# Optimization experiments

Hardware: AMD Instinct MI355X
Metric: run time of the kernel (lower is better)

## Reference

```python
import jax, jax.numpy as jnp
import numpy as np

D_MODEL = 1024
D_FF = 4096
NUM_EXPERTS = 8
TOP_K = 2
B, S = 4, 4096


def setup_inputs() -> dict:
    key = jax.random.key(0)
    ks = jax.random.split(key, 7)
    s_dm = 1.0 / np.sqrt(D_MODEL)
    s_ff = 1.0 / np.sqrt(D_FF)
    return {
        "x": jax.random.normal(ks[0], (B, S, D_MODEL), jnp.float32),
        "router_w": jax.random.normal(ks[1], (D_MODEL, NUM_EXPERTS), jnp.float32) * s_dm,
        "router_b": jnp.zeros((NUM_EXPERTS,), jnp.float32),
        "w1": jax.random.normal(ks[2], (NUM_EXPERTS, D_MODEL, D_FF), jnp.float32) * s_dm,
        "b1": jnp.zeros((NUM_EXPERTS, D_FF), jnp.float32),
        "w2": jax.random.normal(ks[3], (NUM_EXPERTS, D_FF, D_MODEL), jnp.float32) * s_ff,
        "b2": jnp.zeros((NUM_EXPERTS, D_MODEL), jnp.float32),
    }


def reference(x, router_w, router_b, w1, b1, w2, b2):
    Bx, Sx, D = x.shape
    xf = x.reshape(-1, D)  # [T, D], T = B*S
    # Router: top-k logits -> softmax over the k selected experts
    logits = xf @ router_w + router_b            # [T, E]
    top_w, sel = jax.lax.top_k(logits, TOP_K)    # [T, k], [T, k]
    gates = jax.nn.softmax(top_w, axis=-1)       # [T, k]

    def body(i, acc):
        # Dense expert FFN over all tokens; gate is zero for tokens not routed
        # to expert i, which reproduces the masked gather/scatter combine exactly.
        h = jax.nn.gelu(xf @ w1[i] + b1[i], approximate=False)  # [T, d_ff]
        out_i = h @ w2[i] + b2[i]                               # [T, D]
        gate_i = jnp.sum(gates * (sel == i), axis=-1, keepdims=True)  # [T, 1]
        return acc + out_i * gate_i

    out = jax.lax.fori_loop(0, NUM_EXPERTS, body, jnp.zeros_like(xf))
    return out.reshape(Bx, Sx, D)
```

## Files before the change

kernel.cpp:

```cpp
#include <hip/hip_runtime.h>

#define D_MODEL 1024
#define D_FF    4096
#define NE      8
#define T_TOK   16384
#define HOFF    (2u * 1024u * 1024u)

using frag_ab = __attribute__((ext_vector_type(8))) short;
using f32x4   = __attribute__((ext_vector_type(4))) float;
using ushort8 = __attribute__((ext_vector_type(8))) unsigned short;
using ushort4v = __attribute__((ext_vector_type(4))) unsigned short;

__device__ __forceinline__ unsigned short f2bf(float f) {
  unsigned int u = __builtin_bit_cast(unsigned int, f);
  u += 0x7FFFu + ((u >> 16) & 1u);
  return (unsigned short)(u >> 16);
}
__device__ __forceinline__ float bf2f(unsigned short s) {
  unsigned int u = ((unsigned int)s) << 16;
  return __builtin_bit_cast(float, u);
}

__device__ __forceinline__ float gelu_f(float v) {
  float z  = v * 0.70710678118654752f;
  float az = __builtin_fabsf(z);
  float d  = __builtin_fmaf(0.3275911f, az, 1.0f);
  float t;
  asm("v_rcp_f32_e32 %0, %1" : "=v"(t) : "v"(d));
  t = t * (2.0f - d * t);
  float p = __builtin_fmaf(t, 1.061405429f, -1.453152027f);
  p = __builtin_fmaf(t, p, 1.421413741f);
  p = __builtin_fmaf(t, p, -0.284496736f);
  p = __builtin_fmaf(t, p, 0.254829592f);
  p = p * t;
  float ex = __expf(-az * az);
  float er = __builtin_fmaf(-p, ex, 1.0f);
  unsigned int su = __builtin_bit_cast(unsigned int, z) & 0x80000000u;
  er = __builtin_bit_cast(float, __builtin_bit_cast(unsigned int, er) | su);
  return 0.5f * v * (1.0f + er);
}

__device__ __forceinline__ void gload16(const void* g, void* l) {
  __builtin_amdgcn_global_load_lds((const __attribute__((address_space(1))) void*)g,
                                   (__attribute__((address_space(3))) void*)l, 16, 0, 0);
}

#define FENCE __builtin_amdgcn_sched_barrier(0)
#define BARRIER do { FENCE; __builtin_amdgcn_s_barrier(); FENCE; } while (0)
__device__ __forceinline__ void waitv(int n) {
  if (n == 6) asm volatile("s_waitcnt vmcnt(6)" ::: "memory");
  else        asm volatile("s_waitcnt vmcnt(0)" ::: "memory");
}

__global__ __launch_bounds__(256) void router_kernel(
    const float* __restrict__ x, const float* __restrict__ rw,
    const float* __restrict__ rb, int* __restrict__ cnt,
    int* __restrict__ tok, int* __restrict__ mi, float* __restrict__ mg,
    unsigned short* __restrict__ xb) {
  __shared__ int lcnt[NE];
  __shared__ int base[NE];
  __shared__ int lexp[64][2];
  __shared__ int lrank[64][2];
  int w = threadIdx.x >> 6, lane = threadIdx.x & 63;
  if (threadIdx.x < NE) lcnt[threadIdx.x] = 0;
  __syncthreads();

  for (int it = 0; it < 16; ++it) {
    int li = w * 16 + it;
    int t = blockIdx.x * 64 + li;
    const float* xr = x + (size_t)t * D_MODEL;
    unsigned short* xbr = xb + (size_t)t * D_MODEL;
    double acc[NE];
#pragma unroll
    for (int e = 0; e < NE; ++e) acc[e] = 0.0;
#pragma unroll
    for (int it2 = 0; it2 < 4; ++it2) {
      int j = it2 * 256 + lane * 4;
      float4 v = *(const float4*)(xr + j);
      ushort4v o;
      o[0] = f2bf(v.x); o[1] = f2bf(v.y); o[2] = f2bf(v.z); o[3] = f2bf(v.w);
      *(ushort4v*)(xbr + j) = o;
      const float* w0 = rw + (size_t)j * NE;
      const float vv[4] = {v.x, v.y, v.z, v.w};
#pragma unroll
      for (int q = 0; q < 4; ++q) {
        double xv = (double)vv[q];
#pragma unroll
        for (int e = 0; e < NE; ++e) acc[e] += xv * (double)w0[q * NE + e];
      }
    }
#pragma unroll
    for (int e = 0; e < NE; ++e) {
      double v = acc[e];
#pragma unroll
      for (int s = 32; s > 0; s >>= 1) v += __shfl_xor(v, s, 64);
      acc[e] = v;
    }
    if (lane == 0) {
      double lg[NE];
#pragma unroll
      for (int e = 0; e < NE; ++e) lg[e] = acc[e] + (double)rb[e];
      int b0 = 0; double v0 = lg[0];
#pragma unroll
      for (int e = 1; e < NE; ++e) if (lg[e] > v0) { v0 = lg[e]; b0 = e; }
      int b1 = -1; double v1 = -1.0e300;
#pragma unroll
      for (int e = 0; e < NE; ++e) if (e != b0 && lg[e] > v1) { v1 = lg[e]; b1 = e; }
      double g0 = 1.0 / (1.0 + exp(v1 - v0));
      lexp[li][0] = b0; lexp[li][1] = b1;
      lrank[li][0] = atomicAdd(&lcnt[b0], 1);
      lrank[li][1] = atomicAdd(&lcnt[b1], 1);
      mg[2 * t + 0] = (float)g0; mg[2 * t + 1] = (float)(1.0 - g0);
    }
  }
  __syncthreads();
  if (threadIdx.x < NE) base[threadIdx.x] = atomicAdd(&cnt[threadIdx.x], lcnt[threadIdx.x]);
  __syncthreads();
  if (threadIdx.x < 64) {
    int li = threadIdx.x;
    int t = blockIdx.x * 64 + li;
    int e0 = lexp[li][0], e1 = lexp[li][1];
    int p0 = base[e0] + lrank[li][0], p1 = base[e1] + lrank[li][1];
    tok[e0 * T_TOK + p0] = t;
    tok[e1 * T_TOK + p1] = t;
    mi[4 * t + 0] = e0; mi[4 * t + 1] = e1;
    mi[4 * t + 2] = p0; mi[4 * t + 3] = p1;
  }
}

__global__ __launch_bounds__(256) void transpose_cvt_kernel(const float* __restrict__ in,
                                                            unsigned short* __restrict__ out,
                                                            int R, int C) {
  __shared__ unsigned short tile[64][66];
  int e = blockIdx.z;
  int r0 = blockIdx.y * 64, c0 = blockIdx.x * 64;
  int t = threadIdx.x;
  int rr = t >> 4, cc = (t & 15) * 4;
  const float* src = in + ((size_t)e * R + r0) * C + c0;
#pragma unroll
  for (int p = 0; p < 4; ++p) {
    int r = rr + p * 16;
    float4 v = *(const float4*)(src + (size_t)r * C + cc);
    tile[r][cc + 0] = f2bf(v.x);
    tile[r][cc + 1] = f2bf(v.y);
    tile[r][cc + 2] = f2bf(v.z);
    tile[r][cc + 3] = f2bf(v.w);
  }
  __syncthreads();
  int oc = t >> 2, kc = (t & 3) * 16;
  ushort8 v0, v1;
#pragma unroll
  for (int i = 0; i < 8; ++i) v0[i] = tile[kc + i][oc];
#pragma unroll
  for (int i = 0; i < 8; ++i) v1[i] = tile[kc + 8 + i][oc];
  unsigned short* dst = out + ((size_t)e * C + c0 + oc) * R + r0 + kc;
  *(ushort8*)dst = v0;
  *(ushort8*)(dst + 8) = v1;
}

__device__ __forceinline__ int find_tile256(const int* __restrict__ cnt, int slot,
                                            int& e, int& lt, int& ne, int& hb) {
  int tacc = 0, base = 0;
  for (int i = 0; i < NE; ++i) {
    int n = cnt[i];
    int tl = (n + 255) >> 8;
    if (slot < tacc + tl) { e = i; lt = slot - tacc; ne = n; hb = base; return 1; }
    tacc += tl; base += tl << 8;
  }
  return 0;
}

#define STG_A(qa, kt, b) do { \
    gload16(pA##qa##0 + (size_t)(kt) * 64, ldsp + (b) * 65536 + dA + (qa) * 8192); \
    gload16(pA##qa##1 + (size_t)(kt) * 64, ldsp + (b) * 65536 + dA + (qa) * 8192 + 16384); \
  } while (0)
#define STG_B(qb, kt, b) do { \
    gload16(pB##qb##0 + (size_t)(kt) * 64, ldsp + (b) * 65536 + 32768 + dB + (qb) * 4096); \
    gload16(pB##qb##1 + (size_t)(kt) * 64, ldsp + (b) * 65536 + 32768 + dB + (qb) * 4096 + 16384); \
  } while (0)

#define GEMM_BODY(NTILES)                                                        \
  f32x4 acc[8][4] = {};                                                          \
  frag_ab a[4][2], bb[4][2];                                                     \
  const int NT = (NTILES);                                                       \
  STG_A(0, 0, 0); STG_B(0, 0, 0); STG_B(1, 0, 0); STG_A(1, 0, 0);                \
  STG_A(0, 1, 1); STG_B(0, 1, 1); STG_B(1, 1, 1);                                \
  waitv(6); BARRIER;                                                             \
  for (int t = 0; t < NT; ++t) {                                                 \
    const char* AB = ldsp + (t & 1) * 65536;                                     \
    _Pragma("unroll") for (int i = 0; i < 4; ++i) {                              \
      a[i][0] = *(const frag_ab*)(AB + aoff + i * 2048 + xs0);                   \
      a[i][1] = *(const frag_ab*)(AB + aoff + i * 2048 + xs1);                   \
    }                                                                            \
    _Pragma("unroll") for (int j = 0; j < 2; ++j) {                              \
      bb[j][0] = *(const frag_ab*)(AB + boff + j * 2048 + xs0);                  \
      bb[j][1] = *(const frag_ab*)(AB + boff + j * 2048 + xs1);                  \
    }                                                                            \
    if (t + 1 < NT) STG_A(1, t + 1, (t + 1) & 1);                                \
    BARRIER;                                                                     \
    __builtin_amdgcn_s_setprio(1);                                               \
    _Pragma("unroll") for (int i = 0; i < 4; ++i)                                \
      _Pragma("unroll") for (int j = 0; j < 2; ++j) {                            \
        acc[i][j] = __builtin_amdgcn_mfma_f32_16x16x32_bf16(a[i][0], bb[j][0], acc[i][j], 0, 0, 0); \
        acc[i][j] = __builtin_amdgcn_mfma_f32_16x16x32_bf16(a[i][1], bb[j][1], acc[i][j], 0, 0, 0); \
      }                                                                          \
    __builtin_amdgcn_s_setprio(0);                                               \
    BARRIER;                                                                     \
    _Pragma("unroll") for (int j = 0; j < 2; ++j) {                              \
      bb[2 + j][0] = *(const frag_ab*)(AB + boff + (2 + j) * 2048 + xs0);        \
      bb[2 + j][1] = *(const frag_ab*)(AB + boff + (2 + j) * 2048 + xs1);        \
    }                                                                            \
    if (t + 2 < NT) STG_A(0, t + 2, t & 1);                                      \
    BARRIER;                                                                     \
    __builtin_amdgcn_s_setprio(1);                                               \
    _Pragma("unroll") for (int i = 0; i < 4; ++i)                                \
      _Pragma("unroll") for (int j = 0; j < 2; ++j) {                            \
        acc[i][2 + j] = __builtin_amdgcn_mfma_f32_16x16x32_bf16(a[i][0], bb[2 + j][0], acc[i][2 + j], 0, 0, 0); \
        acc[i][2 + j] = __builtin_amdgcn_mfma_f32_16x16x32_bf16(a[i][1], bb[2 + j][1], acc[i][2 + j], 0, 0, 0); \
      }                                                                          \
    __builtin_amdgcn_s_setprio(0);                                               \
    BARRIER;                                                                     \
    _Pragma("unroll") for (int i = 0; i < 4; ++i) {                              \
      a[i][0] = *(const frag_ab*)(AB + aoff + 8192 + i * 2048 + xs0);            \
      a[i][1] = *(const frag_ab*)(AB + aoff + 8192 + i * 2048 + xs1);            \
    }                                                                            \
    if (t + 2 < NT) STG_B(0, t + 2, t & 1);                                      \
    BARRIER;                                                                     \
    __builtin_amdgcn_s_setprio(1);                                               \
    _Pragma("unroll") for (int i = 0; i < 4; ++i)                                \
      _Pragma("unroll") for (int j = 0; j < 2; ++j) {                            \
        acc[4 + i][2 + j] = __builtin_amdgcn_mfma_f32_16x16x32_bf16(a[i][0], bb[2 + j][0], acc[4 + i][2 + j], 0, 0, 0); \
        acc[4 + i][2 + j] = __builtin_amdgcn_mfma_f32_16x16x32_bf16(a[i][1], bb[2 + j][1], acc[4 + i][2 + j], 0, 0, 0); \
      }                                                                          \
    __builtin_amdgcn_s_setprio(0);                                               \
    BARRIER;                                                                     \
    if (t + 2 < NT) STG_B(1, t + 2, t & 1);                                      \
    BARRIER;                                                                     \
    __builtin_amdgcn_s_setprio(1);                                               \
    _Pragma("unroll") for (int i = 0; i < 4; ++i)                                \
      _Pragma("unroll") for (int j = 0; j < 2; ++j) {                            \
        acc[4 + i][j] = __builtin_amdgcn_mfma_f32_16x16x32_bf16(a[i][0], bb[j][0], acc[4 + i][j], 0, 0, 0); \
        acc[4 + i][j] = __builtin_amdgcn_mfma_f32_16x16x32_bf16(a[i][1], bb[j][1], acc[4 + i][j], 0, 0, 0); \
      }                                                                          \
    __builtin_amdgcn_s_setprio(0);                                               \
    waitv((t + 2 < NT) ? 6 : 0);                                                 \
    BARRIER;                                                                     \
  }

__global__ __launch_bounds__(512, 2) void gemm1_kernel(
    const unsigned short* __restrict__ xb, const unsigned short* __restrict__ w1t,
    const float* __restrict__ b1, const int* __restrict__ cnt, const int* __restrict__ tok,
    unsigned short* __restrict__ H) {
  __shared__ __align__(16) char lds[131072];
  int bid = blockIdx.x;
  int s = bid >> 3;
  int tt = (bid & 7) + 8 * (s >> 4);
  int e, lt, ne, hb;
  if (!find_tile256(cnt, tt, e, lt, ne, hb)) return;
  char* ldsp = (char*)lds;
  const int tid = threadIdx.x;
  const int lane = tid & 63, w = tid >> 6;
  const int wm = w >> 2, wn = w & 3;
  const int r16 = lane & 15, kg = lane >> 4;
  const int n0 = (s & 15) * 256;

  const int xs0 = (kg ^ (r16 & 7)) * 16;
  const int xs1 = ((4 + kg) ^ (r16 & 7)) * 16;
  const int aoff = (wm * 128 + r16) * 128;
  const int boff = 32768 + (wn * 64 + r16) * 128;

  const int v = w * 8 + (lane >> 3);
  const int c8off = ((lane & 7) ^ ((lane >> 3) & 7)) * 8;
  const int dA = w * 1024;
  const int dB = (w & 3) * 1024 + (w >> 2) * 8192;
  const int tokbase = e * T_TOK;
  int rA00 = v, rA01 = v + 128, rA10 = 64 + v, rA11 = 192 + v;
  int g00 = lt * 256 + rA00, g01 = lt * 256 + rA01, g10 = lt * 256 + rA10, g11 = lt * 256 + rA11;
  int tk00 = tok[tokbase + ((g00 < ne) ? g00 : 0)];
  int tk01 = tok[tokbase + ((g01 < ne) ? g01 : 0)];
  int tk10 = tok[tokbase + ((g10 < ne) ? g10 : 0)];
  int tk11 = tok[tokbase + ((g11 < ne) ? g11 : 0)];
  const unsigned short* pA00 = xb + (size_t)tk00 * D_MODEL + c8off;
  const unsigned short* pA01 = xb + (size_t)tk01 * D_MODEL + c8off;
  const unsigned short* pA10 = xb + (size_t)tk10 * D_MODEL + c8off;
  const unsigned short* pA11 = xb + (size_t)tk11 * D_MODEL + c8off;
  int rB00 = (v & 31) + (v >> 5) * 64;
  int rB01 = rB00 + 128, rB10 = rB00 + 32, rB11 = rB00 + 160;
  const unsigned short* pB00 = w1t + ((size_t)e * D_FF + n0 + rB00) * D_MODEL + c8off;
  const unsigned short* pB01 = w1t + ((size_t)e * D_FF + n0 + rB01) * D_MODEL + c8off;
  const unsigned short* pB10 = w1t + ((size_t)e * D_FF + n0 + rB10) * D_MODEL + c8off;
  const unsigned short* pB11 = w1t + ((size_t)e * D_FF + n0 + rB11) * D_MODEL + c8off;

  GEMM_BODY(D_MODEL / 64)

  unsigned short (*hlds)[272] = (unsigned short (*)[272])ldsp;
  float b1v[4];
#pragma unroll
  for (int j = 0; j < 4; ++j)
    b1v[j] = b1[e * D_FF + n0 + wn * 64 + j * 16 + r16];
#pragma unroll
  for (int ih = 0; ih < 2; ++ih) {
    if (ih) BARRIER;
#pragma unroll
    for (int i2 = 0; i2 < 4; ++i2)
#pragma unroll
      for (int jj = 0; jj < 4; ++jj) {
        int rl = wm * 64 + i2 * 16 + kg * 4 + jj;
#pragma unroll
        for (int j = 0; j < 4; ++j) {
          int col = wn * 64 + j * 16 + r16;
          int pos = (((col >> 3) ^ (rl & 7)) << 3) | (col & 7);
          hlds[rl][pos] = f2bf(gelu_f(acc[ih * 4 + i2][j][jj] + b1v[j]));
        }
      }
    BARRIER;
    int lrow = tid >> 2, cq = tid & 3;
    int grow = (lrow >> 6) * 128 + ih * 64 + (lrow & 63);
    unsigned short* hdst = H + (size_t)(hb + lt * 256 + grow) * D_FF + n0 + cq * 8;
#pragma unroll
    for (int c = 0; c < 8; ++c) {
      int k = cq + c * 4;
      ushort8 vv = *(const ushort8*)&hlds[lrow][(k ^ (lrow & 7)) << 3];
      __builtin_nontemporal_store(vv, (ushort8*)(hdst + c * 32));
    }
  }
}

__global__ __launch_bounds__(512, 2) void gemm2_kernel(
    const unsigned short* __restrict__ H, const unsigned short* __restrict__ w2t,
    const float* __restrict__ b2, const int* __restrict__ cnt,
    unsigned short* __restrict__ Y) {
  __shared__ __align__(16) char lds[131072];
  int bid = blockIdx.x;
  int s = bid >> 3;
  int tt = (bid & 7) + 8 * (s >> 2);
  int e, lt, ne, hb;
  if (!find_tile256(cnt, tt, e, lt, ne, hb)) return;
  char* ldsp = (char*)lds;
  const int tid = threadIdx.x;
  const int lane = tid & 63, w = tid >> 6;
  const int wm = w >> 2, wn = w & 3;
  const int r16 = lane & 15, kg = lane >> 4;
  const int n0 = (s & 3) * 256;

  const int xs0 = (kg ^ (r16 & 7)) * 16;
  const int xs1 = ((4 + kg) ^ (r16 & 7)) * 16;
  const int aoff = (wm * 128 + r16) * 128;
  const int boff = 32768 + (wn * 64 + r16) * 128;

  const int v = w * 8 + (lane >> 3);
  const int c8off = ((lane & 7) ^ ((lane >> 3) & 7)) * 8;
  const int dA = w * 1024;
  const int dB = (w & 3) * 1024 + (w >> 2) * 8192;
  int rA00 = v, rA01 = v + 128, rA10 = 64 + v, rA11 = 192 + v;
  const unsigned short* pA00 = H + (size_t)(hb + lt * 256 + rA00) * D_FF + c8off;
  const unsigned short* pA01 = H + (size_t)(hb + lt * 256 + rA01) * D_FF + c8off;
  const unsigned short* pA10 = H + (size_t)(hb + lt * 256 + rA10) * D_FF + c8off;
  const unsigned short* pA11 = H + (size_t)(hb + lt * 256 + rA11) * D_FF + c8off;
  int rB00 = (v & 31) + (v >> 5) * 64;
  int rB01 = rB00 + 128, rB10 = rB00 + 32, rB11 = rB00 + 160;
  const unsigned short* pB00 = w2t + ((size_t)e * D_MODEL + n0 + rB00) * D_FF + c8off;
  const unsigned short* pB01 = w2t + ((size_t)e * D_MODEL + n0 + rB01) * D_FF + c8off;
  const unsigned short* pB10 = w2t + ((size_t)e * D_MODEL + n0 + rB10) * D_FF + c8off;
  const unsigned short* pB11 = w2t + ((size_t)e * D_MODEL + n0 + rB11) * D_FF + c8off;

  GEMM_BODY(D_FF / 64)

  unsigned short (*hlds)[272] = (unsigned short (*)[272])ldsp;
  float b2v[4];
#pragma unroll
  for (int j = 0; j < 4; ++j)
    b2v[j] = b2[e * D_MODEL + n0 + wn * 64 + j * 16 + r16];
#pragma unroll
  for (int ih = 0; ih < 2; ++ih) {
    if (ih) BARRIER;
#pragma unroll
    for (int i2 = 0; i2 < 4; ++i2)
#pragma unroll
      for (int jj = 0; jj < 4; ++jj) {
        int rl = wm * 64 + i2 * 16 + kg * 4 + jj;
#pragma unroll
        for (int j = 0; j < 4; ++j) {
          int col = wn * 64 + j * 16 + r16;
          int pos = (((col >> 3) ^ (rl & 7)) << 3) | (col & 7);
          hlds[rl][pos] = f2bf(acc[ih * 4 + i2][j][jj] + b2v[j]);
        }
      }
    BARRIER;
    int lrow = tid >> 2, cq = tid & 3;
    int grow = (lrow >> 6) * 128 + ih * 64 + (lrow & 63);
    unsigned short* ydst = Y + (size_t)(hb + lt * 256 + grow) * D_MODEL + n0 + cq * 8;
#pragma unroll
    for (int c = 0; c < 8; ++c) {
      int k = cq + c * 4;
      ushort8 vv = *(const ushort8*)&hlds[lrow][(k ^ (lrow & 7)) << 3];
      __builtin_nontemporal_store(vv, (ushort8*)(ydst + c * 32));
    }
  }
}

__global__ __launch_bounds__(256) void combine_kernel(
    const unsigned short* __restrict__ Y, const int* __restrict__ cnt,
    const int* __restrict__ mi, const float* __restrict__ mg,
    float* __restrict__ out) {
  int w = threadIdx.x >> 6, lane = threadIdx.x & 63;
  int t = blockIdx.x * 4 + w;
  int e0 = mi[4 * t], e1 = mi[4 * t + 1], p0 = mi[4 * t + 2], p1 = mi[4 * t + 3];
  float g0 = mg[2 * t], g1 = mg[2 * t + 1];
  int hbA = 0, hbB = 0, accv = 0;
#pragma unroll
  for (int e = 0; e < NE; ++e) {
    if (e == e0) hbA = accv;
    if (e == e1) hbB = accv;
    accv += (cnt[e] + 255) & ~255;
  }
  const unsigned short* ra = Y + (size_t)(hbA + p0) * D_MODEL;
  const unsigned short* rb = Y + (size_t)(hbB + p1) * D_MODEL;
  float* orow = out + (size_t)t * D_MODEL;
#pragma unroll
  for (int it = 0; it < 4; ++it) {
    int c = it * 256 + lane * 4;
    ushort4v va = *(const ushort4v*)(ra + c);
    ushort4v vb = *(const ushort4v*)(rb + c);
    f32x4 o;
#pragma unroll
    for (int k = 0; k < 4; ++k) o[k] = g0 * bf2f(va[k]) + g1 * bf2f(vb[k]);
    *(f32x4*)(orow + c) = o;
  }
}

extern "C" void kernel_launch(void* const* d_in, const int* in_sizes, int n_in,
                              void* d_out, int out_size, void* d_ws, size_t ws_size,
                              hipStream_t stream) {
  const float* x  = (const float*)d_in[0];
  const float* rw = (const float*)d_in[1];
  const float* rb = (const float*)d_in[2];
  const float* w1 = (const float*)d_in[3];
  const float* b1 = (const float*)d_in[4];
  const float* w2 = (const float*)d_in[5];
  const float* b2 = (const float*)d_in[6];
  float* out = (float*)d_out;
  char* ws = (char*)d_ws;

  int*   cnt = (int*)ws;
  int*   tok = (int*)(ws + 256);
  int*   mi  = (int*)(ws + 256 + 524288);
  float* mg  = (float*)(ws + 256 + 524288 + 262144);

  unsigned short* xb  = (unsigned short*)(ws + HOFF);
  unsigned short* w1t = (unsigned short*)(ws + HOFF + 33554432u);
  unsigned short* w2t = (unsigned short*)(ws + HOFF + 33554432u + 67108864u);
  unsigned short* H   = (unsigned short*)(ws + HOFF + 33554432u + 67108864u + 67108864u);
  unsigned short* Y   = (unsigned short*)(ws + HOFF);

  hipMemsetAsync(cnt, 0, 64, stream);
  router_kernel<<<dim3(T_TOK / 64), dim3(256), 0, stream>>>(x, rw, rb, cnt, tok, mi, mg, xb);
  transpose_cvt_kernel<<<dim3(D_FF / 64, D_MODEL / 64, NE), dim3(256), 0, stream>>>(w1, w1t, D_MODEL, D_FF);
  transpose_cvt_kernel<<<dim3(D_MODEL / 64, D_FF / 64, NE), dim3(256), 0, stream>>>(w2, w2t, D_FF, D_MODEL);
  gemm1_kernel<<<dim3(8 * 17 * 16), dim3(512), 0, stream>>>(xb, w1t, b1, cnt, tok, H);
  gemm2_kernel<<<dim3(8 * 17 * 4), dim3(512), 0, stream>>>(H, w2t, b2, cnt, Y);
  combine_kernel<<<dim3(T_TOK / 4), dim3(256), 0, stream>>>(Y, cnt, mi, mg, out);
}
```

Baseline: 844.8 us.

## Fuse expert GEMM1 and GEMM2 into one persistent-queue kernel with tile flags

Merges the two expert GEMM launches into one kernel. Blocks take work items from an atomic counter, GEMM1 items first, and each GEMM2 item spins until all 16 GEMM1 column tiles of its token tile have been written. This lets the second GEMM start on finished token tiles while others are still in GEMM1, removing the launch gap and the tail idle between the two kernels. The router also now uses 1024 threads per block with fewer tokens per wave. Occupancy is lowered to one block per CU, and the spin-waits plus fences add overhead and risk stalls if ordering assumptions break.

```diff
diff --git a/kernel.cpp b/kernel.cpp
--- a/kernel.cpp
+++ b/kernel.cpp
@@ -4,6 +4,8 @@
 #define D_FF    4096
 #define NE      8
 #define T_TOK   16384
+#define NG1     2176
+#define NG2     544
 #define HOFF    (2u * 1024u * 1024u)
 
 using frag_ab = __attribute__((ext_vector_type(8))) short;
@@ -52,7 +54,7 @@
   else        asm volatile("s_waitcnt vmcnt(0)" ::: "memory");
 }
 
-__global__ __launch_bounds__(256) void router_kernel(
+__global__ __launch_bounds__(1024) void router_kernel(
     const float* __restrict__ x, const float* __restrict__ rw,
     const float* __restrict__ rb, int* __restrict__ cnt,
     int* __restrict__ tok, int* __restrict__ mi, float* __restrict__ mg,
@@ -65,8 +67,8 @@
   if (threadIdx.x < NE) lcnt[threadIdx.x] = 0;
   __syncthreads();
 
-  for (int it = 0; it < 16; ++it) {
-    int li = w * 16 + it;
+  for (int it = 0; it < 4; ++it) {
+    int li = w * 4 + it;
     int t = blockIdx.x * 64 + li;
     const float* xr = x + (size_t)t * D_MODEL;
     unsigned short* xbr = xb + (size_t)t * D_MODEL;
@@ -247,154 +249,147 @@
     BARRIER;                                                                     \
   }
 
-__global__ __launch_bounds__(512, 2) void gemm1_kernel(
+__global__ __launch_bounds__(512, 1) void moe_fused(
     const unsigned short* __restrict__ xb, const unsigned short* __restrict__ w1t,
-    const float* __restrict__ b1, const int* __restrict__ cnt, const int* __restrict__ tok,
-    unsigned short* __restrict__ H) {
+    const float* __restrict__ b1, const unsigned short* __restrict__ w2t,
+    const float* __restrict__ b2, const int* __restrict__ cnt,
+    const int* __restrict__ tok, unsigned short* __restrict__ H,
+    unsigned short* __restrict__ Y, int* __restrict__ qctr, int* __restrict__ ttdone) {
   __shared__ __align__(16) char lds[131072];
-  int bid = blockIdx.x;
-  int s = bid >> 3;
-  int tt = (bid & 7) + 8 * (s >> 4);
-  int e, lt, ne, hb;
-  if (!find_tile256(cnt, tt, e, lt, ne, hb)) return;
+  __shared__ int item_s;
+  if (threadIdx.x == 0) item_s = atomicAdd(qctr, 1);
+  __syncthreads();
+  const int item = item_s;
   char* ldsp = (char*)lds;
   const int tid = threadIdx.x;
   const int lane = tid & 63, w = tid >> 6;
   const int wm = w >> 2, wn = w & 3;
   const int r16 = lane & 15, kg = lane >> 4;
-  const int n0 = (s & 15) * 256;
-
   const int xs0 = (kg ^ (r16 & 7)) * 16;
   const int xs1 = ((4 + kg) ^ (r16 & 7)) * 16;
   const int aoff = (wm * 128 + r16) * 128;
   const int boff = 32768 + (wn * 64 + r16) * 128;
-
   const int v = w * 8 + (lane >> 3);
   const int c8off = ((lane & 7) ^ ((lane >> 3) & 7)) * 8;
   const int dA = w * 1024;
   const int dB = (w & 3) * 1024 + (w >> 2) * 8192;
-  const int tokbase = e * T_TOK;
-  int rA00 = v, rA01 = v + 128, rA10 = 64 + v, rA11 = 192 + v;
-  int g00 = lt * 256 + rA00, g01 = lt * 256 + rA01, g10 = lt * 256 + rA10, g11 = lt * 256 + rA11;
-  int tk00 = tok[tokbase + ((g00 < ne) ? g00 : 0)];
-  int tk01 = tok[tokbase + ((g01 < ne) ? g01 : 0)];
-  int tk10 = tok[tokbase + ((g10 < ne) ? g10 : 0)];
-  int tk11 = tok[tokbase + ((g11 < ne) ? g11 : 0)];
-  const unsigned short* pA00 = xb + (size_t)tk00 * D_MODEL + c8off;
-  const unsigned short* pA01 = xb + (size_t)tk01 * D_MODEL + c8off;
-  const unsigned short* pA10 = xb + (size_t)tk10 * D_MODEL + c8off;
-  const unsigned short* pA11 = xb + (size_t)tk11 * D_MODEL + c8off;
-  int rB00 = (v & 31) + (v >> 5) * 64;
-  int rB01 = rB00 + 128, rB10 = rB00 + 32, rB11 = rB00 + 160;
-  const unsigned short* pB00 = w1t + ((size_t)e * D_FF + n0 + rB00) * D_MODEL + c8off;
-  const unsigned short* pB01 = w1t + ((size_t)e * D_FF + n0 + rB01) * D_MODEL + c8off;
-  const unsigned short* pB10 = w1t + ((size_t)e * D_FF + n0 + rB10) * D_MODEL + c8off;
-  const unsigned short* pB11 = w1t + ((size_t)e * D_FF + n0 + rB11) * D_MODEL + c8off;
-
-  GEMM_BODY(D_MODEL / 64)
-
-  unsigned short (*hlds)[272] = (unsigned short (*)[272])ldsp;
-  float b1v[4];
-#pragma unroll
-  for (int j = 0; j < 4; ++j)
-    b1v[j] = b1[e * D_FF + n0 + wn * 64 + j * 16 + r16];
-#pragma unroll
-  for (int ih = 0; ih < 2; ++ih) {
-    if (ih) BARRIER;
-#pragma unroll
-    for (int i2 = 0; i2 < 4; ++i2)
-#pragma unroll
-      for (int jj = 0; jj < 4; ++jj) {
-        int rl = wm * 64 + i2 * 16 + kg * 4 + jj;
-#pragma unroll
-        for (int j = 0; j < 4; ++j) {
-          int col = wn * 64 + j * 16 + r16;
-          int pos = (((col >> 3) ^ (rl & 7)) << 3) | (col & 7);
-          hlds[rl][pos] = f2bf(gelu_f(acc[ih * 4 + i2][j][jj] + b1v[j]));
+
+  if (item < NG1) {
+    int s = item >> 3;
+    int tt = (item & 7) + 8 * (s >> 4);
+    int e, lt, ne, hb;
+    if (!find_tile256(cnt, tt, e, lt, ne, hb)) return;
+    const int n0 = (s & 15) * 256;
+    const int tokbase = e * T_TOK;
+    int rA00 = v, rA01 = v + 128, rA10 = 64 + v, rA11 = 192 + v;
+    int g00 = lt * 256 + rA00, g01 = lt * 256 + rA01, g10 = lt * 256 + rA10, g11 = lt * 256 + rA11;
+    int tk00 = tok[tokbase + ((g00 < ne) ? g00 : 0)];
+    int tk01 = tok[tokbase + ((g01 < ne) ? g01 : 0)];
+    int tk10 = tok[tokbase + ((g10 < ne) ? g10 : 0)];
+    int tk11 = tok[tokbase + ((g11 < ne) ? g11 : 0)];
+    const unsigned short* pA00 = xb + (size_t)tk00 * D_MODEL + c8off;
+    const unsigned short* pA01 = xb + (size_t)tk01 * D_MODEL + c8off;
+    const unsigned short* pA10 = xb + (size_t)tk10 * D_MODEL + c8off;
+    const unsigned short* pA11 = xb + (size_t)tk11 * D_MODEL + c8off;
+    int rB00 = (v & 31) + (v >> 5) * 64;
+    int rB01 = rB00 + 128, rB10 = rB00 + 32, rB11 = rB00 + 160;
+    const unsigned short* pB00 = w1t + ((size_t)e * D_FF + n0 + rB00) * D_MODEL + c8off;
+    const unsigned short* pB01 = w1t + ((size_t)e * D_FF + n0 + rB01) * D_MODEL + c8off;
+    const unsigned short* pB10 = w1t + ((size_t)e * D_FF + n0 + rB10) * D_MODEL + c8off;
+    const unsigned short* pB11 = w1t + ((size_t)e * D_FF + n0 + rB11) * D_MODEL + c8off;
+
+    GEMM_BODY(D_MODEL / 64)
+
+    unsigned short (*hlds)[272] = (unsigned short (*)[272])ldsp;
+    float b1v[4];
+#pragma unroll
+    for (int j = 0; j < 4; ++j)
+      b1v[j] = b1[e * D_FF + n0 + wn * 64 + j * 16 + r16];
+#pragma unroll
+    for (int ih = 0; ih < 2; ++ih) {
+      if (ih) BARRIER;
+#pragma unroll
+      for (int i2 = 0; i2 < 4; ++i2)
+#pragma unroll
+        for (int jj = 0; jj < 4; ++jj) {
+          int rl = wm * 64 + i2 * 16 + kg * 4 + jj;
+#pragma unroll
+          for (int j = 0; j < 4; ++j) {
+            int col = wn * 64 + j * 16 + r16;
+            int pos = (((col >> 3) ^ (rl & 7)) << 3) | (col & 7);
+            hlds[rl][pos] = f2bf(gelu_f(acc[ih * 4 + i2][j][jj] + b1v[j]));
+          }
         }
+      BARRIER;
+      int lrow = tid >> 2, cq = tid & 3;
+      int grow = (lrow >> 6) * 128 + ih * 64 + (lrow & 63);
+      unsigned short* hdst = H + (size_t)(hb + lt * 256 + grow) * D_FF + n0 + cq * 8;
+#pragma unroll
+      for (int c = 0; c < 8; ++c) {
+        int k = cq + c * 4;
+        ushort8 vv = *(const ushort8*)&hlds[lrow][(k ^ (lrow & 7)) << 3];
+        __builtin_nontemporal_store(vv, (ushort8*)(hdst + c * 32));
       }
-    BARRIER;
-    int lrow = tid >> 2, cq = tid & 3;
-    int grow = (lrow >> 6) * 128 + ih * 64 + (lrow & 63);
-    unsigned short* hdst = H + (size_t)(hb + lt * 256 + grow) * D_FF + n0 + cq * 8;
-#pragma unroll
-    for (int c = 0; c < 8; ++c) {
-      int k = cq + c * 4;
-      ushort8 vv = *(const ushort8*)&hlds[lrow][(k ^ (lrow & 7)) << 3];
-      __builtin_nontemporal_store(vv, (ushort8*)(hdst + c * 32));
-    }
-  }
-}
-
-__global__ __launch_bounds__(512, 2) void gemm2_kernel(
-    const unsigned short* __restrict__ H, const unsigned short* __restrict__ w2t,
-    const float* __restrict__ b2, const int* __restrict__ cnt,
-    unsigned short* __restrict__ Y) {
-  __shared__ __align__(16) char lds[131072];
-  int bid = blockIdx.x;
-  int s = bid >> 3;
-  int tt = (bid & 7) + 8 * (s >> 2);
-  int e, lt, ne, hb;
-  if (!find_tile256(cnt, tt, e, lt, ne, hb)) return;
-  char* ldsp = (char*)lds;
-  const int tid = threadIdx.x;
-  const int lane = tid & 63, w = tid >> 6;
-  const int wm = w >> 2, wn = w & 3;
-  const int r16 = lane & 15, kg = lane >> 4;
-  const int n0 = (s & 3) * 256;
-
-  const int xs0 = (kg ^ (r16 & 7)) * 16;
-  const int xs1 = ((4 + kg) ^ (r16 & 7)) * 16;
-  const int aoff = (wm * 128 + r16) * 128;
-  const int boff = 32768 + (wn * 64 + r16) * 128;
-
-  const int v = w * 8 + (lane >> 3);
-  const int c8off = ((lane & 7) ^ ((lane >> 3) & 7)) * 8;
-  const int dA = w * 1024;
-  const int dB = (w & 3) * 1024 + (w >> 2) * 8192;
-  int rA00 = v, rA01 = v + 128, rA10 = 64 + v, rA11 = 192 + v;
-  const unsigned short* pA00 = H + (size_t)(hb + lt * 256 + rA00) * D_FF + c8off;
-  const unsigned short* pA01 = H + (size_t)(hb + lt * 256 + rA01) * D_FF + c8off;
-  const unsigned short* pA10 = H + (size_t)(hb + lt * 256 + rA10) * D_FF + c8off;
-  const unsigned short* pA11 = H + (size_t)(hb + lt * 256 + rA11) * D_FF + c8off;
-  int rB00 = (v & 31) + (v >> 5) * 64;
-  int rB01 = rB00 + 128, rB10 = rB00 + 32, rB11 = rB00 + 160;
-  const unsigned short* pB00 = w2t + ((size_t)e * D_MODEL + n0 + rB00) * D_FF + c8off;
-  const unsigned short* pB01 = w2t + ((size_t)e * D_MODEL + n0 + rB01) * D_FF + c8off;
-  const unsigned short* pB10 = w2t + ((size_t)e * D_MODEL + n0 + rB10) * D_FF + c8off;
-  const unsigned short* pB11 = w2t + ((size_t)e * D_MODEL + n0 + rB11) * D_FF + c8off;
-
-  GEMM_BODY(D_FF / 64)
-
-  unsigned short (*hlds)[272] = (unsigned short (*)[272])ldsp;
-  float b2v[4];
-#pragma unroll
-  for (int j = 0; j < 4; ++j)
-    b2v[j] = b2[e * D_MODEL + n0 + wn * 64 + j * 16 + r16];
-#pragma unroll
-  for (int ih = 0; ih < 2; ++ih) {
-    if (ih) BARRIER;
-#pragma unroll
-    for (int i2 = 0; i2 < 4; ++i2)
-#pragma unroll
-      for (int jj = 0; jj < 4; ++jj) {
-        int rl = wm * 64 + i2 * 16 + kg * 4 + jj;
-#pragma unroll
-        for (int j = 0; j < 4; ++j) {
-          int col = wn * 64 + j * 16 + r16;
-          int pos = (((col >> 3) ^ (rl & 7)) << 3) | (col & 7);
-          hlds[rl][pos] = f2bf(acc[ih * 4 + i2][j][jj] + b2v[j]);
+    }
+    __threadfence();
+    __syncthreads();
+    if (tid == 0) atomicAdd(&ttdone[tt], 1);
+  } else {
+    int bid = item - NG1;
+    int s = bid >> 3;
+    int tt = (bid & 7) + 8 * (s >> 2);
+    int e, lt, ne, hb;
+    if (!find_tile256(cnt, tt, e, lt, ne, hb)) return;
+    if (tid == 0) {
+      while (__hip_atomic_load(&ttdone[tt], __ATOMIC_ACQUIRE, __HIP_MEMORY_SCOPE_AGENT) < 16)
+        __builtin_amdgcn_s_sleep(8);
+    }
+    __syncthreads();
+    const int n0 = (s & 3) * 256;
+    int rA00 = v, rA01 = v + 128, rA10 = 64 + v, rA11 = 192 + v;
+    const unsigned short* pA00 = H + (size_t)(hb + lt * 256 + rA00) * D_FF + c8off;
+    const unsigned short* pA01 = H + (size_t)(hb + lt * 256 + rA01) * D_FF + c8off;
+    const unsigned short* pA10 = H + (size_t)(hb + lt * 256 + rA10) * D_FF + c8off;
+    const unsigned short* pA11 = H + (size_t)(hb + lt * 256 + rA11) * D_FF + c8off;
+    int rB00 = (v & 31) + (v >> 5) * 64;
+    int rB01 = rB00 + 128, rB10 = rB00 + 32, rB11 = rB00 + 160;
+    const unsigned short* pB00 = w2t + ((size_t)e * D_MODEL + n0 + rB00) * D_FF + c8off;
+    const unsigned short* pB01 = w2t + ((size_t)e * D_MODEL + n0 + rB01) * D_FF + c8off;
+    const unsigned short* pB10 = w2t + ((size_t)e * D_MODEL + n0 + rB10) * D_FF + c8off;
+    const unsigned short* pB11 = w2t + ((size_t)e * D_MODEL + n0 + rB11) * D_FF + c8off;
+
+    GEMM_BODY(D_FF / 64)
+
+    unsigned short (*hlds)[272] = (unsigned short (*)[272])ldsp;
+    float b2v[4];
+#pragma unroll
+    for (int j = 0; j < 4; ++j)
+      b2v[j] = b2[e * D_MODEL + n0 + wn * 64 + j * 16 + r16];
+#pragma unroll
+    for (int ih = 0; ih < 2; ++ih) {
+      if (ih) BARRIER;
+#pragma unroll
+      for (int i2 = 0; i2 < 4; ++i2)
+#pragma unroll
+        for (int jj = 0; jj < 4; ++jj) {
+          int rl = wm * 64 + i2 * 16 + kg * 4 + jj;
+#pragma unroll
+          for (int j = 0; j < 4; ++j) {
+            int col = wn * 64 + j * 16 + r16;
+            int pos = (((col >> 3) ^ (rl & 7)) << 3) | (col & 7);
+            hlds[rl][pos] = f2bf(acc[ih * 4 + i2][j][jj] + b2v[j]);
+          }
         }
+      BARRIER;
+      int lrow = tid >> 2, cq = tid & 3;
+      int grow = (lrow >> 6) * 128 + ih * 64 + (lrow & 63);
+      unsigned short* ydst = Y + (size_t)(hb + lt * 256 + grow) * D_MODEL + n0 + cq * 8;
+#pragma unroll
+      for (int c = 0; c < 8; ++c) {
+        int k = cq + c * 4;
+        ushort8 vv = *(const ushort8*)&hlds[lrow][(k ^ (lrow & 7)) << 3];
+        __builtin_nontemporal_store(vv, (ushort8*)(ydst + c * 32));
       }
-    BARRIER;
-    int lrow = tid >> 2, cq = tid & 3;
-    int grow = (lrow >> 6) * 128 + ih * 64 + (lrow & 63);
-    unsigned short* ydst = Y + (size_t)(hb + lt * 256 + grow) * D_MODEL + n0 + cq * 8;
-#pragma unroll
-    for (int c = 0; c < 8; ++c) {
-      int k = cq + c * 4;
-      ushort8 vv = *(const ushort8*)&hlds[lrow][(k ^ (lrow & 7)) << 3];
-      __builtin_nontemporal_store(vv, (ushort8*)(ydst + c * 32));
     }
   }
 }
@@ -442,10 +437,12 @@
   float* out = (float*)d_out;
   char* ws = (char*)d_ws;
 
-  int*   cnt = (int*)ws;
-  int*   tok = (int*)(ws + 256);
-  int*   mi  = (int*)(ws + 256 + 524288);
-  float* mg  = (float*)(ws + 256 + 524288 + 262144);
+  int*   qctr   = (int*)ws;
+  int*   ttdone = (int*)(ws + 64);
+  int*   cnt    = (int*)(ws + 1024);
+  int*   tok    = (int*)(ws + 4096);
+  int*   mi     = (int*)(ws + 4096 + 524288);
+  float* mg     = (float*)(ws + 4096 + 524288 + 262144);
 
   unsigned short* xb  = (unsigned short*)(ws + HOFF);
   unsigned short* w1t = (unsigned short*)(ws + HOFF + 33554432u);
@@ -453,11 +450,10 @@
   unsigned short* H   = (unsigned short*)(ws + HOFF + 33554432u + 67108864u + 67108864u);
   unsigned short* Y   = (unsigned short*)(ws + HOFF);
 
-  hipMemsetAsync(cnt, 0, 64, stream);
-  router_kernel<<<dim3(T_TOK / 64), dim3(256), 0, stream>>>(x, rw, rb, cnt, tok, mi, mg, xb);
+  hipMemsetAsync(ws, 0, 4096, stream);
+  router_kernel<<<dim3(T_TOK / 64), dim3(1024), 0, stream>>>(x, rw, rb, cnt, tok, mi, mg, xb);
   transpose_cvt_kernel<<<dim3(D_FF / 64, D_MODEL / 64, NE), dim3(256), 0, stream>>>(w1, w1t, D_MODEL, D_FF);
   transpose_cvt_kernel<<<dim3(D_MODEL / 64, D_FF / 64, NE), dim3(256), 0, stream>>>(w2, w2t, D_FF, D_MODEL);
-  gemm1_kernel<<<dim3(8 * 17 * 16), dim3(512), 0, stream>>>(xb, w1t, b1, cnt, tok, H);
-  gemm2_kernel<<<dim3(8 * 17 * 4), dim3(512), 0, stream>>>(H, w2t, b2, cnt, Y);
+  moe_fused<<<dim3(NG1 + NG2), dim3(512), 0, stream>>>(xb, w1t, b1, w2t, b2, cnt, tok, H, Y, qctr, ttdone);
   combine_kernel<<<dim3(T_TOK / 4), dim3(256), 0, stream>>>(Y, cnt, mi, mg, out);
 }
```

Measured after the change: 1.600 ms. 89.4% more time.
